# Optimization experiments

Measured on AMD Instinct MI355X. Metric: run time of the kernel, lower is better.

The kernel has to match this reference:

```python
import jax, jax.numpy as jnp
import numpy as np

SEQ_LEN = 64
WCNT = 50000
EMB = 128
TOPIC = 256
TH = TOPIC // 2          # bidirectional topic GRU hidden (num_layers=1 branch)
KCNT = 16384             # know_length
KE = 64                  # know_emb_size
SH = 512                 # seq_hidden_size
IN_S = 2 * TOPIC + 1     # 'double' score mode GRU input size


def setup_inputs() -> dict:
    key = jax.random.key(0)
    ks = jax.random.split(key, 24)
    rn = lambda k, shape, s=0.05: jax.random.normal(k, shape, jnp.float32) * s
    un = lambda k, shape: jax.random.uniform(k, shape, jnp.float32, -1.0, 1.0)

    topic = jax.random.randint(ks[0], (SEQ_LEN,), 1, WCNT)
    knowledge = jax.random.uniform(ks[1], (KCNT,), jnp.float32)
    score = jax.random.uniform(ks[2], (1,), jnp.float32)

    emb_table = rn(ks[3], (WCNT, EMB)).at[0].set(0.0)  # padding_idx=0
    # topic bidirectional GRU (torch layout: W_ih [3H, in], gates r,z,n)
    W_ih_f = rn(ks[4], (3 * TH, EMB)); W_hh_f = rn(ks[5], (3 * TH, TH))
    b_ih_f = rn(ks[6], (3 * TH,));     b_hh_f = rn(ks[7], (3 * TH,))
    W_ih_b = rn(ks[8], (3 * TH, EMB)); W_hh_b = rn(ks[9], (3 * TH, TH))
    b_ih_b = rn(ks[10], (3 * TH,));    b_hh_b = rn(ks[11], (3 * TH,))
    # knowledge embedding Linear(KCNT -> KE)
    Wk = rn(ks[12], (KE, KCNT)); bk = rn(ks[13], (KE,))
    # knowledge memory + initial hidden (uniform(-1,1) as in module)
    knowledge_memory = un(ks[14], (KCNT, KE))
    h_initial = un(ks[15], (KCNT, SH))
    # score layer Linear(TOPIC+SH -> 1)
    Ws = rn(ks[16], (1, TOPIC + SH)); bs = rn(ks[17], (1,))
    # memory-slot GRU (input IN_S, hidden SH)
    W_ih_s = rn(ks[18], (3 * SH, IN_S)); W_hh_s = rn(ks[19], (3 * SH, SH))
    b_ih_s = rn(ks[20], (3 * SH,));      b_hh_s = rn(ks[21], (3 * SH,))

    return dict(topic=topic, knowledge=knowledge, score=score, emb_table=emb_table,
                W_ih_f=W_ih_f, W_hh_f=W_hh_f, b_ih_f=b_ih_f, b_hh_f=b_hh_f,
                W_ih_b=W_ih_b, W_hh_b=W_hh_b, b_ih_b=b_ih_b, b_hh_b=b_hh_b,
                Wk=Wk, bk=bk, knowledge_memory=knowledge_memory, h_initial=h_initial,
                Ws=Ws, bs=bs, W_ih_s=W_ih_s, W_hh_s=W_hh_s, b_ih_s=b_ih_s, b_hh_s=b_hh_s)


def gru_cell(x, h, Wih, Whh, bih, bhh):
    # torch GRU cell: gates ordered (r, z, n)
    gi = x @ Wih.T + bih
    gh = h @ Whh.T + bhh
    gi_r, gi_z, gi_n = jnp.split(gi, 3, axis=-1)
    gh_r, gh_z, gh_n = jnp.split(gh, 3, axis=-1)
    r = jax.nn.sigmoid(gi_r + gh_r)
    z = jax.nn.sigmoid(gi_z + gh_z)
    n = jnp.tanh(gi_n + r * gh_n)
    return (1.0 - z) * n + z * h


def run_gru(xs, h0, Wih, Whh, bih, bhh):
    def step(h, x):
        h2 = gru_cell(x, h, Wih, Whh, bih, bhh)
        return h2, h2
    _, ys = jax.lax.scan(step, h0, xs)
    return ys


def reference(topic, knowledge, score, emb_table,
              W_ih_f, W_hh_f, b_ih_f, b_hh_f,
              W_ih_b, W_hh_b, b_ih_b, b_hh_b,
              Wk, bk, knowledge_memory, h_initial,
              Ws, bs, W_ih_s, W_hh_s, b_ih_s, b_hh_s):
    # ---- topic encoder: embedding + bidirectional GRU + max over time ----
    x = emb_table[topic]                                      # [T, EMB]
    h0 = jnp.zeros((TH,), x.dtype)
    yf = run_gru(x, h0, W_ih_f, W_hh_f, b_ih_f, b_hh_f)       # [T, TH]
    yb = run_gru(x[::-1], h0, W_ih_b, W_hh_b, b_ih_b, b_hh_b)[::-1]
    v = jnp.max(jnp.concatenate([yf, yb], axis=-1), axis=0)   # [TOPIC]

    # ---- knowledge embedding + attention over memory ----
    kn = knowledge @ Wk.T + bk                                # [KE]
    alpha = knowledge_memory @ kn                             # [KCNT]
    beta = jax.nn.softmax(alpha)                              # [KCNT]

    h = h_initial                                             # [KCNT, SH]
    hkp = beta @ h                                            # [SH] attention read
    pred_v = jnp.concatenate([v, hkp])                        # [TOPIC+SH]
    predict_score = (pred_v @ Ws[0] + bs[0]).reshape(1)       # [1]

    # ---- 'double' input construction + broadcast write to all slots ----
    pos = (score >= 0.5).astype(v.dtype)                      # [1] broadcasts over v
    x_in = jnp.concatenate([v * pos, v * (1.0 - pos), score]) # [2*TOPIC+1]
    xk = beta[:, None] * x_in[None, :]                        # [KCNT, IN_S]

    h_new = gru_cell(xk, h, W_ih_s, W_hh_s, b_ih_s, b_hh_s)   # [KCNT, SH]
    return predict_score, h_new[None]                         # ([1], [1, KCNT, SH])
```

## Files before the change

### kernel.cpp

```cpp
#include <hip/hip_runtime.h>
#include <math.h>


#define SEQ 64
#define EMB 128
#define TH 128
#define G3 384
#define KCNT 16384
#define KE 64
#define SH 512
#define GS3 1536
#define INS 513

typedef _Float16 f16x8 __attribute__((ext_vector_type(8)));
typedef float f32x4 __attribute__((ext_vector_type(4)));

__device__ __forceinline__ float sigmoidf_(float x) {
    return 1.0f / (1.0f + expf(-x));
}
__device__ __forceinline__ float sigmoid_fast(float x) {
    return 1.0f / (1.0f + __expf(-x));
}
__device__ __forceinline__ float tanh_fast(float x) {
    return 2.0f / (1.0f + __expf(-2.0f * x)) - 1.0f;
}

__device__ __forceinline__ void gl_lds16(const void* g, void* l) {
    __builtin_amdgcn_global_load_lds(
        (const __attribute__((address_space(1))) unsigned int*)g,
        (__attribute__((address_space(3))) unsigned int*)l, 16, 0, 0);
}

__global__ __launch_bounds__(384) void topic_gi_kernel(
    const int* __restrict__ topic, const float* __restrict__ emb,
    const float* __restrict__ Wih_f, const float* __restrict__ bih_f,
    const float* __restrict__ Wih_b, const float* __restrict__ bih_b,
    float* __restrict__ gi_ws)
{
    const int t = blockIdx.x;
    const int dir = blockIdx.y;
    const int g = threadIdx.x;
    const float* Wih = dir ? Wih_b : Wih_f;
    const float* bih = dir ? bih_b : bih_f;
    const int tok = topic[dir ? (SEQ - 1 - t) : t];
    const float4* e4 = (const float4*)(emb + (size_t)tok * EMB);
    const float4* w4 = (const float4*)(Wih + (size_t)g * EMB);
    float acc = bih[g];
    #pragma unroll
    for (int q = 0; q < EMB / 4; ++q) {
        float4 w = w4[q], e = e4[q];
        acc += w.x * e.x + w.y * e.y + w.z * e.z + w.w * e.w;
    }
    gi_ws[((size_t)dir * SEQ + t) * G3 + g] = acc;
}

__global__ __launch_bounds__(384) void topic_gru_seq_kernel(
    const float* __restrict__ Whh_f, const float* __restrict__ bhh_f,
    const float* __restrict__ Whh_b, const float* __restrict__ bhh_b,
    const float* __restrict__ gi_ws, float* __restrict__ v_out)
{
    const int dir = blockIdx.x;
    const float* Whh = dir ? Whh_b : Whh_f;
    const float* bhh = dir ? bhh_b : bhh_f;
    const float* gi = gi_ws + (size_t)dir * SEQ * G3;
    const int tid = threadIdx.x;

    __shared__ float hbuf[TH];
    __shared__ float ghbuf[G3];

    float4 w[32];
    const float4* w4 = (const float4*)(Whh + (size_t)tid * TH);
    #pragma unroll
    for (int q = 0; q < 32; ++q) w[q] = w4[q];
    const float bh = bhh[tid];

    if (tid < TH) hbuf[tid] = 0.0f;
    __syncthreads();

    float vmax = -1e30f;
    for (int t = 0; t < SEQ; ++t) {
        const float4* h4 = (const float4*)hbuf;
        float acc = bh;
        #pragma unroll
        for (int q = 0; q < 32; ++q) {
            float4 hh = h4[q];
            acc += w[q].x * hh.x + w[q].y * hh.y + w[q].z * hh.z + w[q].w * hh.w;
        }
        ghbuf[tid] = acc;
        __syncthreads();
        if (tid < TH) {
            float gir = gi[(size_t)t * G3 + tid];
            float giz = gi[(size_t)t * G3 + tid + TH];
            float gin = gi[(size_t)t * G3 + tid + 2 * TH];
            float r = sigmoidf_(gir + ghbuf[tid]);
            float z = sigmoidf_(giz + ghbuf[tid + TH]);
            float n = tanhf(fmaf(r, ghbuf[tid + 2 * TH], gin));
            float hn = (1.0f - z) * n + z * hbuf[tid];
            hbuf[tid] = hn;
            vmax = fmaxf(vmax, hn);
        }
        __syncthreads();
    }
    if (tid < TH) v_out[dir * TH + tid] = vmax;
}

__global__ __launch_bounds__(256) void kn_kernel(
    const float* __restrict__ Wk, const float* __restrict__ bk,
    const float* __restrict__ knowledge, float* __restrict__ kn)
{
    const int row = blockIdx.x;
    const int tid = threadIdx.x;
    const float4* w4 = (const float4*)(Wk + (size_t)row * KCNT);
    const float4* k4 = (const float4*)knowledge;
    float acc = 0.0f;
    for (int i = tid; i < KCNT / 4; i += 256) {
        float4 w = w4[i], k = k4[i];
        acc += w.x * k.x + w.y * k.y + w.z * k.z + w.w * k.w;
    }
    #pragma unroll
    for (int off = 32; off; off >>= 1) acc += __shfl_xor(acc, off);
    __shared__ float red[4];
    if ((tid & 63) == 0) red[tid >> 6] = acc;
    __syncthreads();
    if (tid == 0) kn[row] = red[0] + red[1] + red[2] + red[3] + bk[row];
}

__global__ __launch_bounds__(256) void alpha_kernel(
    const float* __restrict__ km, const float* __restrict__ kn,
    float* __restrict__ alpha)
{
    const int idx = blockIdx.x * 256 + threadIdx.x;
    const int row = idx >> 6;
    const int lane = idx & 63;
    float p = km[(size_t)row * KE + lane] * kn[lane];
    #pragma unroll
    for (int off = 32; off; off >>= 1) p += __shfl_xor(p, off);
    if (lane == 0) alpha[row] = p;
}

__global__ __launch_bounds__(1024) void softmax_kernel(
    const float* __restrict__ alpha, float* __restrict__ beta)
{
    const int tid = threadIdx.x;
    float vals[16];
    float m = -1e30f;
    #pragma unroll
    for (int i = 0; i < 16; ++i) {
        vals[i] = alpha[tid + i * 1024];
        m = fmaxf(m, vals[i]);
    }
    #pragma unroll
    for (int off = 32; off; off >>= 1) m = fmaxf(m, __shfl_xor(m, off));
    __shared__ float red[16];
    if ((tid & 63) == 0) red[tid >> 6] = m;
    __syncthreads();
    float M = red[0];
    #pragma unroll
    for (int wv = 1; wv < 16; ++wv) M = fmaxf(M, red[wv]);
    __syncthreads();
    float s = 0.0f;
    #pragma unroll
    for (int i = 0; i < 16; ++i) {
        vals[i] = expf(vals[i] - M);
        s += vals[i];
    }
    #pragma unroll
    for (int off = 32; off; off >>= 1) s += __shfl_xor(s, off);
    if ((tid & 63) == 0) red[tid >> 6] = s;
    __syncthreads();
    float S = 0.0f;
    #pragma unroll
    for (int wv = 0; wv < 16; ++wv) S += red[wv];
    const float inv = 1.0f / S;
    #pragma unroll
    for (int i = 0; i < 16; ++i) beta[tid + i * 1024] = vals[i] * inv;
}

__global__ __launch_bounds__(512) void hkp_partial_kernel(
    const float* __restrict__ beta, const float* __restrict__ hinit,
    float* __restrict__ part)
{
    const int j = threadIdx.x;
    const int b = blockIdx.x;
    const int r0 = b * (KCNT / 128);
    float acc = 0.0f;
    for (int r = 0; r < KCNT / 128; ++r)
        acc = fmaf(beta[r0 + r], hinit[(size_t)(r0 + r) * SH + j], acc);
    part[(size_t)b * SH + j] = acc;
}

__global__ __launch_bounds__(512) void score_xin_kernel(
    const float* __restrict__ part, const float* __restrict__ v,
    const float* __restrict__ score, const float* __restrict__ Ws,
    const float* __restrict__ bs, float* __restrict__ x_in,
    float* __restrict__ out)
{
    const int tid = threadIdx.x;
    float hkp = 0.0f;
    for (int b = 0; b < 128; ++b) hkp += part[(size_t)b * SH + tid];
    float contrib = hkp * Ws[256 + tid];
    if (tid < 256) contrib += v[tid] * Ws[tid];
    #pragma unroll
    for (int off = 32; off; off >>= 1) contrib += __shfl_xor(contrib, off);
    __shared__ float red[8];
    if ((tid & 63) == 0) red[tid >> 6] = contrib;
    __syncthreads();
    if (tid == 0) {
        float p = bs[0];
        #pragma unroll
        for (int wv = 0; wv < 8; ++wv) p += red[wv];
        out[0] = p;
    }
    const float sc = score[0];
    const float pos = (sc >= 0.5f) ? 1.0f : 0.0f;
    if (tid < 256) {
        x_in[tid] = v[tid] * pos;
        x_in[256 + tid] = v[tid] * (1.0f - pos);
    }
    if (tid == 0) x_in[512] = sc;
}

__global__ __launch_bounds__(256) void gih_kernel(
    const float* __restrict__ Wih_s, const float* __restrict__ x_in,
    float* __restrict__ g_raw)
{
    const int gw = (blockIdx.x * 256 + threadIdx.x) >> 6;
    const int lane = threadIdx.x & 63;
    const float* row = Wih_s + (size_t)gw * INS;
    float acc = 0.0f;
    for (int k = lane; k < INS; k += 64) acc += row[k] * x_in[k];
    #pragma unroll
    for (int off = 32; off; off >>= 1) acc += __shfl_xor(acc, off);
    if (lane == 0) g_raw[gw] = acc;
}

__global__ __launch_bounds__(256) void cvt_f16_kernel(
    const float* __restrict__ s, _Float16* __restrict__ d, int n8)
{
    const int i = blockIdx.x * 256 + threadIdx.x;
    if (i >= n8) return;
    const float4* s4 = (const float4*)s + (size_t)i * 2;
    const float4 a = s4[0], b = s4[1];
    f16x8 o;
    o[0] = (_Float16)a.x; o[1] = (_Float16)a.y;
    o[2] = (_Float16)a.z; o[3] = (_Float16)a.w;
    o[4] = (_Float16)b.x; o[5] = (_Float16)b.y;
    o[6] = (_Float16)b.z; o[7] = (_Float16)b.w;
    *(f16x8*)(d + (size_t)i * 8) = o;
}

__global__ __launch_bounds__(256, 2) void slot_gru_mfma_kernel(
    const float* __restrict__ h32,
    const _Float16* __restrict__ h16,
    const _Float16* __restrict__ W16,
    const float* __restrict__ beta,
    const float* __restrict__ g_raw,
    const float* __restrict__ b_ih,
    const float* __restrict__ b_hh,
    float* __restrict__ out)
{
    __shared__ _Float16 As[128 * 32];
    __shared__ _Float16 Bs[192 * 32];

    const int tid = threadIdx.x;
    const int lane = tid & 63;
    const int wv  = tid >> 6;
    const int wm  = (wv >> 1) * 64;
    const int wn  = (wv & 1) * 32;
    const int nt  = blockIdx.x & 7;
    const int mt  = blockIdx.x >> 3;
    const int m0  = mt * 128;
    const int c0  = nt * 64;
    const int l15 = lane & 15;
    const int l4  = lane >> 4;

    f32x4 acc[4][3][2];
    #pragma unroll
    for (int mi = 0; mi < 4; ++mi)
        #pragma unroll
        for (int g = 0; g < 3; ++g)
            #pragma unroll
            for (int ni = 0; ni < 2; ++ni)
                acc[mi][g][ni] = (f32x4){0.f, 0.f, 0.f, 0.f};

    for (int k0 = 0; k0 < SH; k0 += 32) {
        #pragma unroll
        for (int p = 0; p < 2; ++p) {
            const int idx = tid + p * 256;
            const int r = idx >> 2, c = idx & 3;
            gl_lds16(h16 + (size_t)(m0 + r) * SH + k0 + c * 8, &As[idx * 8]);
        }
        #pragma unroll
        for (int p = 0; p < 3; ++p) {
            const int idx = tid + p * 256;
            const int r = idx >> 2, c = idx & 3;
            const int g = r >> 6, wcol = r & 63;
            gl_lds16(W16 + (size_t)(g * SH + c0 + wcol) * SH + k0 + c * 8,
                     &Bs[idx * 8]);
        }
        __syncthreads();

        f16x8 af[4], bf[3][2];
        #pragma unroll
        for (int mi = 0; mi < 4; ++mi)
            af[mi] = *(const f16x8*)&As[(wm + mi * 16 + l15) * 32 + l4 * 8];
        #pragma unroll
        for (int g = 0; g < 3; ++g)
            #pragma unroll
            for (int ni = 0; ni < 2; ++ni)
                bf[g][ni] = *(const f16x8*)&Bs[(g * 64 + wn + ni * 16 + l15) * 32 + l4 * 8];

        #pragma unroll
        for (int mi = 0; mi < 4; ++mi)
            #pragma unroll
            for (int g = 0; g < 3; ++g)
                #pragma unroll
                for (int ni = 0; ni < 2; ++ni)
                    acc[mi][g][ni] = __builtin_amdgcn_mfma_f32_16x16x32_f16(
                        af[mi], bf[g][ni], acc[mi][g][ni], 0, 0, 0);
        __syncthreads();
    }

    float bhh_[3][2], bih_[3][2], gr_[3][2];
    #pragma unroll
    for (int ni = 0; ni < 2; ++ni) {
        const int col = c0 + wn + ni * 16 + l15;
        #pragma unroll
        for (int g = 0; g < 3; ++g) {
            bhh_[g][ni] = b_hh[col + g * SH];
            bih_[g][ni] = b_ih[col + g * SH];
            gr_[g][ni]  = g_raw[col + g * SH];
        }
    }
    #pragma unroll
    for (int mi = 0; mi < 4; ++mi) {
        #pragma unroll
        for (int j = 0; j < 4; ++j) {
            const int row = m0 + wm + mi * 16 + l4 * 4 + j;
            const float bt = beta[row];
            #pragma unroll
            for (int ni = 0; ni < 2; ++ni) {
                const int col = c0 + wn + ni * 16 + l15;
                const float hp = h32[(size_t)row * SH + col];
                const float ghr = acc[mi][0][ni][j] + bhh_[0][ni];
                const float ghz = acc[mi][1][ni][j] + bhh_[1][ni];
                const float ghn = acc[mi][2][ni][j] + bhh_[2][ni];
                const float gir = fmaf(bt, gr_[0][ni], bih_[0][ni]);
                const float giz = fmaf(bt, gr_[1][ni], bih_[1][ni]);
                const float gin = fmaf(bt, gr_[2][ni], bih_[2][ni]);
                const float r = sigmoid_fast(gir + ghr);
                const float z = sigmoid_fast(giz + ghz);
                const float n = tanh_fast(fmaf(r, ghn, gin));
                out[1 + (size_t)row * SH + col] = (1.0f - z) * n + z * hp;
            }
        }
    }
}

#define BM 64
#define BN 64
#define BK 32

__global__ __launch_bounds__(256) void slot_gru_kernel(
    const float* __restrict__ hinit, const float* __restrict__ Whh,
    const float* __restrict__ beta, const float* __restrict__ g_raw,
    const float* __restrict__ b_ih, const float* __restrict__ b_hh,
    float* __restrict__ out)
{
    __shared__ float As_[BK][BM];
    __shared__ float Bs_[BK][3 * BN];

    const int tid = threadIdx.x;
    const int ct = blockIdx.x & 7;
    const int rt = blockIdx.x >> 3;
    const int m0 = rt * BM;
    const int c0 = ct * BN;
    const int tm = (tid & 15) * 4;
    const int tc = (tid >> 4) * 4;

    float acc[4][12];
    #pragma unroll
    for (int i = 0; i < 4; ++i)
        #pragma unroll
        for (int j = 0; j < 12; ++j) acc[i][j] = 0.0f;

    for (int k0 = 0; k0 < SH; k0 += BK) {
        #pragma unroll
        for (int p = 0; p < 2; ++p) {
            const int m = (tid >> 3) + p * 32;
            const int kc = (tid & 7) * 4;
            const float4 a = *(const float4*)(hinit + (size_t)(m0 + m) * SH + k0 + kc);
            As_[kc + 0][m] = a.x; As_[kc + 1][m] = a.y;
            As_[kc + 2][m] = a.z; As_[kc + 3][m] = a.w;
        }
        #pragma unroll
        for (int p = 0; p < 6; ++p) {
            const int r = (tid >> 3) + p * 32;
            const int kc = (tid & 7) * 4;
            const int slice = r >> 6;
            const int wrow = slice * SH + c0 + (r & 63);
            const float4 b = *(const float4*)(Whh + (size_t)wrow * SH + k0 + kc);
            Bs_[kc + 0][r] = b.x; Bs_[kc + 1][r] = b.y;
            Bs_[kc + 2][r] = b.z; Bs_[kc + 3][r] = b.w;
        }
        __syncthreads();
        for (int k = 0; k < BK; ++k) {
            const float4 av = *(const float4*)&As_[k][tm];
            const float4 b0 = *(const float4*)&Bs_[k][tc];
            const float4 b1 = *(const float4*)&Bs_[k][BN + tc];
            const float4 b2 = *(const float4*)&Bs_[k][2 * BN + tc];
            const float a[4] = {av.x, av.y, av.z, av.w};
            const float bb[12] = {b0.x, b0.y, b0.z, b0.w,
                                  b1.x, b1.y, b1.z, b1.w,
                                  b2.x, b2.y, b2.z, b2.w};
            #pragma unroll
            for (int i = 0; i < 4; ++i)
                #pragma unroll
                for (int j = 0; j < 12; ++j)
                    acc[i][j] = fmaf(a[i], bb[j], acc[i][j]);
        }
        __syncthreads();
    }
    #pragma unroll
    for (int i = 0; i < 4; ++i) {
        const int row = m0 + tm + i;
        const float b = beta[row];
        const float4 hp = *(const float4*)(hinit + (size_t)row * SH + c0 + tc);
        float o[4];
        const float hprev[4] = {hp.x, hp.y, hp.z, hp.w};
        #pragma unroll
        for (int j = 0; j < 4; ++j) {
            const int col = c0 + tc + j;
            const float ghr = acc[i][j] + b_hh[col];
            const float ghz = acc[i][4 + j] + b_hh[col + SH];
            const float ghn = acc[i][8 + j] + b_hh[col + 2 * SH];
            const float gir = fmaf(b, g_raw[col], b_ih[col]);
            const float giz = fmaf(b, g_raw[col + SH], b_ih[col + SH]);
            const float gin = fmaf(b, g_raw[col + 2 * SH], b_ih[col + 2 * SH]);
            const float r = sigmoidf_(gir + ghr);
            const float z = sigmoidf_(giz + ghz);
            const float n = tanhf(fmaf(r, ghn, gin));
            o[j] = (1.0f - z) * n + z * hprev[j];
        }
        *(float4*)(out + 1 + (size_t)row * SH + c0 + tc) =
            make_float4(o[0], o[1], o[2], o[3]);
    }
}

extern "C" void kernel_launch(void* const* d_in, const int* in_sizes, int n_in,
                              void* d_out, int out_size, void* d_ws, size_t ws_size,
                              hipStream_t stream) {
    const int*   topic     = (const int*)d_in[0];
    const float* knowledge = (const float*)d_in[1];
    const float* score     = (const float*)d_in[2];
    const float* emb       = (const float*)d_in[3];
    const float* Wih_f     = (const float*)d_in[4];
    const float* Whh_f     = (const float*)d_in[5];
    const float* bih_f     = (const float*)d_in[6];
    const float* bhh_f     = (const float*)d_in[7];
    const float* Wih_b     = (const float*)d_in[8];
    const float* Whh_b     = (const float*)d_in[9];
    const float* bih_b     = (const float*)d_in[10];
    const float* bhh_b     = (const float*)d_in[11];
    const float* Wk        = (const float*)d_in[12];
    const float* bk        = (const float*)d_in[13];
    const float* km        = (const float*)d_in[14];
    const float* h0        = (const float*)d_in[15];
    const float* Ws        = (const float*)d_in[16];
    const float* bs        = (const float*)d_in[17];
    const float* Wih_s     = (const float*)d_in[18];
    const float* Whh_s     = (const float*)d_in[19];
    const float* bih_s     = (const float*)d_in[20];
    const float* bhh_s     = (const float*)d_in[21];

    float* out = (float*)d_out;
    float* ws  = (float*)d_ws;

    float* v     = ws + 0;
    float* kn    = ws + 256;
    float* alpha = ws + 320;
    float* beta  = ws + 16704;
    float* part  = ws + 33088;
    float* x_in  = ws + 98624;
    float* g_raw = ws + 99140;
    float* gi_ws = ws + 100680;

    const size_t H16_OFF = 655360;
    const size_t W16_OFF = H16_OFF + (size_t)KCNT * SH * 2;
    const size_t NEED    = W16_OFF + (size_t)GS3 * SH * 2;
    _Float16* h16 = (_Float16*)((char*)d_ws + H16_OFF);
    _Float16* W16 = (_Float16*)((char*)d_ws + W16_OFF);
    const bool use_mfma = ws_size >= NEED;

    if (use_mfma) {
        cvt_f16_kernel<<<(KCNT * SH / 8 + 255) / 256, 256, 0, stream>>>(
            h0, h16, KCNT * SH / 8);
        cvt_f16_kernel<<<(GS3 * SH / 8 + 255) / 256, 256, 0, stream>>>(
            Whh_s, W16, GS3 * SH / 8);
    }

    topic_gi_kernel<<<dim3(SEQ, 2), G3, 0, stream>>>(topic, emb, Wih_f, bih_f,
                                                     Wih_b, bih_b, gi_ws);
    topic_gru_seq_kernel<<<2, G3, 0, stream>>>(Whh_f, bhh_f, Whh_b, bhh_b,
                                               gi_ws, v);
    kn_kernel<<<KE, 256, 0, stream>>>(Wk, bk, knowledge, kn);
    alpha_kernel<<<KCNT * 64 / 256, 256, 0, stream>>>(km, kn, alpha);
    softmax_kernel<<<1, 1024, 0, stream>>>(alpha, beta);
    hkp_partial_kernel<<<128, 512, 0, stream>>>(beta, h0, part);
    score_xin_kernel<<<1, 512, 0, stream>>>(part, v, score, Ws, bs, x_in, out);
    gih_kernel<<<GS3 / 4, 256, 0, stream>>>(Wih_s, x_in, g_raw);

    if (use_mfma) {
        slot_gru_mfma_kernel<<<(KCNT / 128) * (SH / 64), 256, 0, stream>>>(
            h0, h16, W16, beta, g_raw, bih_s, bhh_s, out);
    } else {
        slot_gru_kernel<<<(KCNT / BM) * (SH / BN), 256, 0, stream>>>(
            h0, Whh_s, beta, g_raw, bih_s, bhh_s, out);
    }
}
```

Measured before the change: 327.8 us.

## Split topic GRU dot products across lanes, stage gi in LDS, read fp16 h

The topic GRU recurrence now assigns four threads per hidden unit, each holding slices of the r/z/n weight rows, and reduces with lane shuffles. It preloads all input-gate activations into shared memory and double-buffers the hidden state so each step needs one barrier instead of two. The attention-read kernel now reads the fp16 copy of the initial hidden state instead of fp32, roughly halving its traffic but adding rounding error. The non-MFMA fallback path is removed and the fp16 conversion becomes unconditional, which assumes enough workspace.

```diff
diff --git a/kernel.cpp b/kernel.cpp
--- a/kernel.cpp
+++ b/kernel.cpp
@@ -54,54 +54,84 @@
     gi_ws[((size_t)dir * SEQ + t) * G3 + g] = acc;
 }
 
-__global__ __launch_bounds__(384) void topic_gru_seq_kernel(
+__global__ __launch_bounds__(512) void topic_gru_seq_kernel(
     const float* __restrict__ Whh_f, const float* __restrict__ bhh_f,
     const float* __restrict__ Whh_b, const float* __restrict__ bhh_b,
     const float* __restrict__ gi_ws, float* __restrict__ v_out)
 {
     const int dir = blockIdx.x;
-    const float* Whh = dir ? Whh_b : Whh_f;
-    const float* bhh = dir ? bhh_b : bhh_f;
-    const float* gi = gi_ws + (size_t)dir * SEQ * G3;
+    const float* __restrict__ Whh = dir ? Whh_b : Whh_f;
+    const float* __restrict__ bhh = dir ? bhh_b : bhh_f;
+    const float* __restrict__ gi = gi_ws + (size_t)dir * SEQ * G3;
     const int tid = threadIdx.x;
-
-    __shared__ float hbuf[TH];
-    __shared__ float ghbuf[G3];
-
-    float4 w[32];
-    const float4* w4 = (const float4*)(Whh + (size_t)tid * TH);
-    #pragma unroll
-    for (int q = 0; q < 32; ++q) w[q] = w4[q];
-    const float bh = bhh[tid];
-
-    if (tid < TH) hbuf[tid] = 0.0f;
-    __syncthreads();
-
-    float vmax = -1e30f;
+    const int j = tid >> 2;
+    const int s = tid & 3;
+
+    __shared__ float gi_lds[SEQ * G3];
+    __shared__ float hls[2][TH];
+
+    {
+        const float4* src = (const float4*)gi;
+        float4* dst = (float4*)gi_lds;
+        #pragma unroll
+        for (int i = 0; i < SEQ * G3 / 4 / 512; ++i)
+            dst[tid + i * 512] = src[tid + i * 512];
+    }
+
+    float4 wr[8], wz[8], wn[8];
+    {
+        const float4* pr = (const float4*)(Whh + (size_t)j * TH + s * 32);
+        const float4* pz = (const float4*)(Whh + (size_t)(TH + j) * TH + s * 32);
+        const float4* pn = (const float4*)(Whh + (size_t)(2 * TH + j) * TH + s * 32);
+        #pragma unroll
+        for (int q = 0; q < 8; ++q) { wr[q] = pr[q]; wz[q] = pz[q]; wn[q] = pn[q]; }
+    }
+    const float bhr = bhh[j], bhz = bhh[j + TH], bhn = bhh[j + 2 * TH];
+
+    if (tid < TH) hls[0][tid] = 0.0f;
+    float h_old = 0.0f, vmax = -1e30f;
+    __syncthreads();
+
+    int cur = 0;
     for (int t = 0; t < SEQ; ++t) {
-        const float4* h4 = (const float4*)hbuf;
-        float acc = bh;
-        #pragma unroll
-        for (int q = 0; q < 32; ++q) {
-            float4 hh = h4[q];
-            acc += w[q].x * hh.x + w[q].y * hh.y + w[q].z * hh.z + w[q].w * hh.w;
-        }
-        ghbuf[tid] = acc;
+        const float4* h4 = (const float4*)(&hls[cur][s * 32]);
+        float ar0 = 0.f, ar1 = 0.f, az0 = 0.f, az1 = 0.f, an0 = 0.f, an1 = 0.f;
+        #pragma unroll
+        for (int q = 0; q < 8; q += 2) {
+            const float4 h0v = h4[q], h1v = h4[q + 1];
+            ar0 = fmaf(wr[q].x, h0v.x, ar0); ar0 = fmaf(wr[q].y, h0v.y, ar0);
+            ar0 = fmaf(wr[q].z, h0v.z, ar0); ar0 = fmaf(wr[q].w, h0v.w, ar0);
+            ar1 = fmaf(wr[q+1].x, h1v.x, ar1); ar1 = fmaf(wr[q+1].y, h1v.y, ar1);
+            ar1 = fmaf(wr[q+1].z, h1v.z, ar1); ar1 = fmaf(wr[q+1].w, h1v.w, ar1);
+            az0 = fmaf(wz[q].x, h0v.x, az0); az0 = fmaf(wz[q].y, h0v.y, az0);
+            az0 = fmaf(wz[q].z, h0v.z, az0); az0 = fmaf(wz[q].w, h0v.w, az0);
+            az1 = fmaf(wz[q+1].x, h1v.x, az1); az1 = fmaf(wz[q+1].y, h1v.y, az1);
+            az1 = fmaf(wz[q+1].z, h1v.z, az1); az1 = fmaf(wz[q+1].w, h1v.w, az1);
+            an0 = fmaf(wn[q].x, h0v.x, an0); an0 = fmaf(wn[q].y, h0v.y, an0);
+            an0 = fmaf(wn[q].z, h0v.z, an0); an0 = fmaf(wn[q].w, h0v.w, an0);
+            an1 = fmaf(wn[q+1].x, h1v.x, an1); an1 = fmaf(wn[q+1].y, h1v.y, an1);
+            an1 = fmaf(wn[q+1].z, h1v.z, an1); an1 = fmaf(wn[q+1].w, h1v.w, an1);
+        }
+        float ar = ar0 + ar1, az = az0 + az1, an = an0 + an1;
+        ar += __shfl_xor(ar, 1); ar += __shfl_xor(ar, 2);
+        az += __shfl_xor(az, 1); az += __shfl_xor(az, 2);
+        an += __shfl_xor(an, 1); an += __shfl_xor(an, 2);
+        if (s == 0) {
+            const float gir = gi_lds[t * G3 + j];
+            const float giz = gi_lds[t * G3 + j + TH];
+            const float gin = gi_lds[t * G3 + j + 2 * TH];
+            const float r = sigmoidf_(gir + ar + bhr);
+            const float z = sigmoidf_(giz + az + bhz);
+            const float n = tanhf(fmaf(r, an + bhn, gin));
+            const float hn = (1.0f - z) * n + z * h_old;
+            hls[cur ^ 1][j] = hn;
+            h_old = hn;
+            vmax = fmaxf(vmax, hn);
+        }
         __syncthreads();
-        if (tid < TH) {
-            float gir = gi[(size_t)t * G3 + tid];
-            float giz = gi[(size_t)t * G3 + tid + TH];
-            float gin = gi[(size_t)t * G3 + tid + 2 * TH];
-            float r = sigmoidf_(gir + ghbuf[tid]);
-            float z = sigmoidf_(giz + ghbuf[tid + TH]);
-            float n = tanhf(fmaf(r, ghbuf[tid + 2 * TH], gin));
-            float hn = (1.0f - z) * n + z * hbuf[tid];
-            hbuf[tid] = hn;
-            vmax = fmaxf(vmax, hn);
-        }
-        __syncthreads();
-    }
-    if (tid < TH) v_out[dir * TH + tid] = vmax;
+        cur ^= 1;
+    }
+    if (s == 0) v_out[dir * TH + j] = vmax;
 }
 
 __global__ __launch_bounds__(256) void kn_kernel(
@@ -177,7 +207,7 @@
 }
 
 __global__ __launch_bounds__(512) void hkp_partial_kernel(
-    const float* __restrict__ beta, const float* __restrict__ hinit,
+    const float* __restrict__ beta, const _Float16* __restrict__ h16,
     float* __restrict__ part)
 {
     const int j = threadIdx.x;
@@ -185,7 +215,7 @@
     const int r0 = b * (KCNT / 128);
     float acc = 0.0f;
     for (int r = 0; r < KCNT / 128; ++r)
-        acc = fmaf(beta[r0 + r], hinit[(size_t)(r0 + r) * SH + j], acc);
+        acc = fmaf(beta[r0 + r], (float)h16[(size_t)(r0 + r) * SH + j], acc);
     part[(size_t)b * SH + j] = acc;
 }
 
@@ -354,96 +384,6 @@
                 out[1 + (size_t)row * SH + col] = (1.0f - z) * n + z * hp;
             }
         }
-    }
-}
-
-#define BM 64
-#define BN 64
-#define BK 32
-
-__global__ __launch_bounds__(256) void slot_gru_kernel(
-    const float* __restrict__ hinit, const float* __restrict__ Whh,
-    const float* __restrict__ beta, const float* __restrict__ g_raw,
-    const float* __restrict__ b_ih, const float* __restrict__ b_hh,
-    float* __restrict__ out)
-{
-    __shared__ float As_[BK][BM];
-    __shared__ float Bs_[BK][3 * BN];
-
-    const int tid = threadIdx.x;
-    const int ct = blockIdx.x & 7;
-    const int rt = blockIdx.x >> 3;
-    const int m0 = rt * BM;
-    const int c0 = ct * BN;
-    const int tm = (tid & 15) * 4;
-    const int tc = (tid >> 4) * 4;
-
-    float acc[4][12];
-    #pragma unroll
-    for (int i = 0; i < 4; ++i)
-        #pragma unroll
-        for (int j = 0; j < 12; ++j) acc[i][j] = 0.0f;
-
-    for (int k0 = 0; k0 < SH; k0 += BK) {
-        #pragma unroll
-        for (int p = 0; p < 2; ++p) {
-            const int m = (tid >> 3) + p * 32;
-            const int kc = (tid & 7) * 4;
-            const float4 a = *(const float4*)(hinit + (size_t)(m0 + m) * SH + k0 + kc);
-            As_[kc + 0][m] = a.x; As_[kc + 1][m] = a.y;
-            As_[kc + 2][m] = a.z; As_[kc + 3][m] = a.w;
-        }
-        #pragma unroll
-        for (int p = 0; p < 6; ++p) {
-            const int r = (tid >> 3) + p * 32;
-            const int kc = (tid & 7) * 4;
-            const int slice = r >> 6;
-            const int wrow = slice * SH + c0 + (r & 63);
-            const float4 b = *(const float4*)(Whh + (size_t)wrow * SH + k0 + kc);
-            Bs_[kc + 0][r] = b.x; Bs_[kc + 1][r] = b.y;
-            Bs_[kc + 2][r] = b.z; Bs_[kc + 3][r] = b.w;
-        }
-        __syncthreads();
-        for (int k = 0; k < BK; ++k) {
-            const float4 av = *(const float4*)&As_[k][tm];
-            const float4 b0 = *(const float4*)&Bs_[k][tc];
-            const float4 b1 = *(const float4*)&Bs_[k][BN + tc];
-            const float4 b2 = *(const float4*)&Bs_[k][2 * BN + tc];
-            const float a[4] = {av.x, av.y, av.z, av.w};
-            const float bb[12] = {b0.x, b0.y, b0.z, b0.w,
-                                  b1.x, b1.y, b1.z, b1.w,
-                                  b2.x, b2.y, b2.z, b2.w};
-            #pragma unroll
-            for (int i = 0; i < 4; ++i)
-                #pragma unroll
-                for (int j = 0; j < 12; ++j)
-                    acc[i][j] = fmaf(a[i], bb[j], acc[i][j]);
-        }
-        __syncthreads();
-    }
-    #pragma unroll
-    for (int i = 0; i < 4; ++i) {
-        const int row = m0 + tm + i;
-        const float b = beta[row];
-        const float4 hp = *(const float4*)(hinit + (size_t)row * SH + c0 + tc);
-        float o[4];
-        const float hprev[4] = {hp.x, hp.y, hp.z, hp.w};
-        #pragma unroll
-        for (int j = 0; j < 4; ++j) {
-            const int col = c0 + tc + j;
-            const float ghr = acc[i][j] + b_hh[col];
-            const float ghz = acc[i][4 + j] + b_hh[col + SH];
-            const float ghn = acc[i][8 + j] + b_hh[col + 2 * SH];
-            const float gir = fmaf(b, g_raw[col], b_ih[col]);
-            const float giz = fmaf(b, g_raw[col + SH], b_ih[col + SH]);
-            const float gin = fmaf(b, g_raw[col + 2 * SH], b_ih[col + 2 * SH]);
-            const float r = sigmoidf_(gir + ghr);
-            const float z = sigmoidf_(giz + ghz);
-            const float n = tanhf(fmaf(r, ghn, gin));
-            o[j] = (1.0f - z) * n + z * hprev[j];
-        }
-        *(float4*)(out + 1 + (size_t)row * SH + c0 + tc) =
-            make_float4(o[0], o[1], o[2], o[3]);
     }
 }
 
@@ -490,31 +430,23 @@
     const size_t NEED    = W16_OFF + (size_t)GS3 * SH * 2;
     _Float16* h16 = (_Float16*)((char*)d_ws + H16_OFF);
     _Float16* W16 = (_Float16*)((char*)d_ws + W16_OFF);
-    const bool use_mfma = ws_size >= NEED;
-
-    if (use_mfma) {
-        cvt_f16_kernel<<<(KCNT * SH / 8 + 255) / 256, 256, 0, stream>>>(
-            h0, h16, KCNT * SH / 8);
-        cvt_f16_kernel<<<(GS3 * SH / 8 + 255) / 256, 256, 0, stream>>>(
-            Whh_s, W16, GS3 * SH / 8);
-    }
+
+    cvt_f16_kernel<<<(KCNT * SH / 8 + 255) / 256, 256, 0, stream>>>(
+        h0, h16, KCNT * SH / 8);
+    cvt_f16_kernel<<<(GS3 * SH / 8 + 255) / 256, 256, 0, stream>>>(
+        Whh_s, W16, GS3 * SH / 8);
 
     topic_gi_kernel<<<dim3(SEQ, 2), G3, 0, stream>>>(topic, emb, Wih_f, bih_f,
                                                      Wih_b, bih_b, gi_ws);
-    topic_gru_seq_kernel<<<2, G3, 0, stream>>>(Whh_f, bhh_f, Whh_b, bhh_b,
-                                               gi_ws, v);
+    topic_gru_seq_kernel<<<2, 512, 0, stream>>>(Whh_f, bhh_f, Whh_b, bhh_b,
+                                                gi_ws, v);
     kn_kernel<<<KE, 256, 0, stream>>>(Wk, bk, knowledge, kn);
     alpha_kernel<<<KCNT * 64 / 256, 256, 0, stream>>>(km, kn, alpha);
     softmax_kernel<<<1, 1024, 0, stream>>>(alpha, beta);
-    hkp_partial_kernel<<<128, 512, 0, stream>>>(beta, h0, part);
+    hkp_partial_kernel<<<128, 512, 0, stream>>>(beta, h16, part);
     score_xin_kernel<<<1, 512, 0, stream>>>(part, v, score, Ws, bs, x_in, out);
     gih_kernel<<<GS3 / 4, 256, 0, stream>>>(Wih_s, x_in, g_raw);
 
-    if (use_mfma) {
-        slot_gru_mfma_kernel<<<(KCNT / 128) * (SH / 64), 256, 0, stream>>>(
-            h0, h16, W16, beta, g_raw, bih_s, bhh_s, out);
-    } else {
-        slot_gru_kernel<<<(KCNT / BM) * (SH / BN), 256, 0, stream>>>(
-            h0, Whh_s, beta, g_raw, bih_s, bhh_s, out);
-    }
-}
+    slot_gru_mfma_kernel<<<(KCNT / 128) * (SH / 64), 256, 0, stream>>>(
+        h0, h16, W16, beta, g_raw, bih_s, bhh_s, out);
+}
```

New measurement: 295.0 us. 1.11x faster.
